# Kernel tuning notes

Hardware: AMD Instinct MI355X
Metric: run time of the kernel (lower is better)

The kernel has to match this reference:

```python
import jax, jax.numpy as jnp
import numpy as np

S = 7
M = 8        # ensemble size (num_models)
D = 1008     # AEV feature dim
N = 50400    # total atoms (single conformer), divisible by S
LAYER_DIMS = (1008, 256, 192, 160, 1)
CELU_ALPHA = 0.1


def setup_inputs() -> dict:
    key = jax.random.key(0)
    ks = jax.random.split(key, 2 + 2 * (len(LAYER_DIMS) - 1))
    # Equal-size species groups (7200 atoms per species), randomly permuted.
    sp = jnp.tile(jnp.arange(S, dtype=jnp.int32), N // S)
    sp = jax.random.permutation(ks[0], sp)[None, :]                 # [1, N]
    aev = jax.random.normal(ks[1], (1, N, D), dtype=jnp.float32)    # [1, N, D]
    inp = {"species": sp, "aev": aev}
    for i in range(len(LAYER_DIMS) - 1):
        fan_in, fan_out = LAYER_DIMS[i], LAYER_DIMS[i + 1]
        w = jax.random.normal(ks[2 + 2 * i], (S, M, fan_in, fan_out), jnp.float32) / np.float32(np.sqrt(fan_in))
        b = jax.random.normal(ks[3 + 2 * i], (S, M, 1, fan_out), jnp.float32) * 0.01
        inp[f"W{i}"] = w
        inp[f"b{i}"] = b
    return inp


def _celu(x, alpha=CELU_ALPHA):
    return jnp.where(x > 0, x, alpha * jnp.expm1(x / alpha))


def _forward(species, aev, Ws, bs):
    sp = species.reshape(-1)                         # [N]
    x = aev.reshape(-1, aev.shape[-1])               # [N, D]
    s = Ws[0].shape[0]
    n = sp.shape[0]
    g = n // s                                       # atoms per species (equal groups)
    # MoE dispatch: stable sort by species -> contiguous equal-size blocks.
    order = jnp.argsort(sp)                          # [N]
    h = x[order].reshape(s, g, -1)                   # [S, G, D]
    # Fused per-species ensemble MLP (grouped batched GEMM = baddbmm per species).
    h = jnp.einsum('sgd,smdh->smgh', h, Ws[0]) + bs[0]   # [S, M, G, H0]
    for w, b in zip(Ws[1:], bs[1:]):
        h = _celu(h)
        h = jnp.einsum('smgh,smhp->smgp', h, w) + b
    atom_e = jnp.mean(h, axis=1)                     # mean over ensemble -> [S, G, 1]
    # Combine: scatter-sum of per-atom energies -> single molecular energy.
    return jnp.sum(atom_e).reshape(1)


def reference(species, aev, W0, b0, W1, b1, W2, b2, W3, b3):
    return _forward(species, aev, (W0, W1, W2, W3), (b0, b1, b2, b3))
```

## Files before the change

### kernel.cpp

```cpp
#include <hip/hip_runtime.h>
#include <cstdint>
#include <cstddef>

typedef unsigned short u16t;
typedef __attribute__((ext_vector_type(8))) short short8;
typedef __attribute__((ext_vector_type(4))) float float4v;

#define NATOMS 50400
#define SSP    7
#define DIN    1008
#define KP     1024
#define GRP    7200
#define GPAD   7296
#define H0D    256
#define H1D    192
#define H2D    160
#define GBSM   28

#define OFF_CNT   0ull
#define OFF_SRC   256ull
#define OFF_X     204544ull
#define OFF_W0T   104800000ull
#define OFF_W1T   134160128ull
#define OFF_W2T   139665152ull
#define OFF_H0    143105792ull

__device__ __forceinline__ u16t f2bf(float f) {
    union { float f; unsigned u; } x; x.f = f;
    unsigned r = x.u + 0x7fffu + ((x.u >> 16) & 1u);
    return (u16t)(r >> 16);
}
__device__ __forceinline__ float bf2f(u16t h) {
    return __uint_as_float(((unsigned)h) << 16);
}
__device__ __forceinline__ float celu_f(float x) {
    return x > 0.f ? x : 0.1f * (__expf(x * 10.f) - 1.f);
}
__device__ __forceinline__ void gll16(const void* g, void* l) {
    __builtin_amdgcn_global_load_lds(
        (const __attribute__((address_space(1))) void*)g,
        (__attribute__((address_space(3))) void*)l, 16, 0, 0);
}


__global__ void assign_k(const int* __restrict__ sp, int* __restrict__ cnt,
                         int* __restrict__ src_of) {
    int i = blockIdx.x * 256 + threadIdx.x;
    int lane = threadIdx.x & 63;
    int s = (i < NATOMS) ? sp[i] : -1;
#pragma unroll
    for (int t = 0; t < SSP; ++t) {
        unsigned long long m = __ballot(s == t);
        if (s == t) {
            int leader = __ffsll((unsigned long long)m) - 1;
            int rank = __popcll(m & ((1ull << lane) - 1ull));
            int base = 0;
            if (lane == leader) base = atomicAdd(&cnt[t], __popcll(m));
            base = __shfl(base, leader);
            src_of[t * GPAD + base + rank] = i;
        }
    }
}

__global__ void gather_k(const float* __restrict__ aev, const int* __restrict__ src_of,
                         u16t* __restrict__ X) {
    int wv = threadIdx.x >> 6, lane = threadIdx.x & 63;
    int s = blockIdx.y;
    int r = blockIdx.x * 4 + wv;
    int b = s * GPAD + r;
    bool valid = (r < GRP);
    int src = valid ? src_of[b] : 0;
    const float* ap = aev + (size_t)src * DIN;
    u16t* xp = X + (size_t)b * KP;
#pragma unroll
    for (int j = 0; j < 4; ++j) {
        int idx = j * 64 + lane;
        int c = idx * 4;
        ushort4 o; o.x = 0; o.y = 0; o.z = 0; o.w = 0;
        if (valid && c < DIN) {
            float4 v = *(const float4*)(ap + c);
            o.x = f2bf(v.x); o.y = f2bf(v.y); o.z = f2bf(v.z); o.w = f2bf(v.w);
        }
        *(ushort4*)(xp + c) = o;
    }
}

__global__ void transpose_convert_k(const float* __restrict__ src, u16t* __restrict__ dst,
                                    int K_in, int C, int K_out) {
    __shared__ float tile[64][65];
    int b = blockIdx.z;
    int k0 = blockIdx.x * 64, c0 = blockIdx.y * 64;
    int tx = threadIdx.x & 63, ty = threadIdx.x >> 6;
    const float* sp = src + (size_t)b * K_in * C;
#pragma unroll
    for (int i = 0; i < 16; ++i) {
        int kl = i * 4 + ty;
        int k = k0 + kl, c = c0 + tx;
        float v = (k < K_in && c < C) ? sp[(size_t)k * C + c] : 0.f;
        tile[kl][tx] = v;
    }
    __syncthreads();
    u16t* dp = dst + (size_t)b * C * K_out;
#pragma unroll
    for (int i = 0; i < 16; ++i) {
        int cl = i * 4 + ty;
        int c = c0 + cl, k = k0 + tx;
        if (c < C && k < K_out)
            dp[(size_t)c * K_out + k] = f2bf(tile[tx][cl]);
    }
}

__launch_bounds__(256, 2)
__global__ void gemm1(const u16t* __restrict__ X, const u16t* __restrict__ W0T,
                      const float* __restrict__ b0, u16t* __restrict__ H0, int bsm0) {
    __shared__ __attribute__((aligned(16))) char lA[16384];
    __shared__ __attribute__((aligned(16))) char lB[32768];

    const int tid = threadIdx.x, w = tid >> 6, lane = tid & 63;
    const int l15 = lane & 15, quad = lane >> 4;
    const int mtile = blockIdx.x >> 1, ntile = blockIdx.x & 1;
    const int by = blockIdx.y;
    const int bsm = bsm0 + by * 2;
    const int s = bsm >> 3;
    const int wr = w & 1, wc = w >> 1;

    const u16t* Xp  = X + ((size_t)s * GPAD + (size_t)mtile * 128) * KP;
    const u16t* Wp0 = W0T + ((size_t)bsm * H0D + (size_t)ntile * 128) * KP;
    const u16t* Wp1 = W0T + ((size_t)(bsm + 1) * H0D + (size_t)ntile * 128) * KP;

    const u16t* gA[4]; const u16t* gB0[4]; const u16t* gB1[4];
#pragma unroll
    for (int j = 0; j < 4; ++j) {
        int u = j * 256 + w * 64 + lane;
        int r = u >> 3;
        int cs = (u & 7) ^ (r & 7);
        size_t off = (size_t)r * KP + cs * 8;
        gA[j]  = Xp  + off;
        gB0[j] = Wp0 + off;
        gB1[j] = Wp1 + off;
    }
    int aoff[4][2], boff[4][2];
#pragma unroll
    for (int rt = 0; rt < 4; ++rt) {
        int r = wr * 64 + rt * 16 + l15;
        int c = wc * 64 + rt * 16 + l15;
#pragma unroll
        for (int ks = 0; ks < 2; ++ks) {
            aoff[rt][ks] = r * 128 + (((ks * 4 + quad) ^ (r & 7)) * 16);
            boff[rt][ks] = c * 128 + (((ks * 4 + quad) ^ (c & 7)) * 16);
        }
    }

    float4v acc[2][4][4];
#pragma unroll
    for (int m = 0; m < 2; ++m)
#pragma unroll
        for (int i = 0; i < 4; ++i)
#pragma unroll
            for (int j = 0; j < 4; ++j) acc[m][i][j] = (float4v){0.f, 0.f, 0.f, 0.f};

    for (int kt = 0; kt < 16; ++kt) {
        const int ko = kt * 64;
        __syncthreads();
#pragma unroll
        for (int j = 0; j < 4; ++j) {
            gll16(gA[j]  + ko, lA + j * 4096 + w * 1024);
            gll16(gB0[j] + ko, lB + j * 4096 + w * 1024);
            gll16(gB1[j] + ko, lB + 16384 + j * 4096 + w * 1024);
        }
        __syncthreads();
#pragma unroll
        for (int ks = 0; ks < 2; ++ks) {
            short8 a[4], b0f[4], b1f[4];
#pragma unroll
            for (int rt = 0; rt < 4; ++rt) a[rt] = *(const short8*)(lA + aoff[rt][ks]);
#pragma unroll
            for (int ct = 0; ct < 4; ++ct) {
                b0f[ct] = *(const short8*)(lB + boff[ct][ks]);
                b1f[ct] = *(const short8*)(lB + 16384 + boff[ct][ks]);
            }
#pragma unroll
            for (int rt = 0; rt < 4; ++rt)
#pragma unroll
                for (int ct = 0; ct < 4; ++ct) {
                    acc[0][rt][ct] = __builtin_amdgcn_mfma_f32_16x16x32_bf16(a[rt], b0f[ct], acc[0][rt][ct], 0, 0, 0);
                    acc[1][rt][ct] = __builtin_amdgcn_mfma_f32_16x16x32_bf16(a[rt], b1f[ct], acc[1][rt][ct], 0, 0, 0);
                }
        }
    }

#pragma unroll
    for (int m = 0; m < 2; ++m) {
        float bias[4];
#pragma unroll
        for (int ct = 0; ct < 4; ++ct)
            bias[ct] = b0[(bsm + m) * H0D + ntile * 128 + wc * 64 + ct * 16 + l15];
        u16t* Hp = H0 + (size_t)(by * 2 + m) * GPAD * H0D;
#pragma unroll
        for (int rt = 0; rt < 4; ++rt)
#pragma unroll
            for (int ct = 0; ct < 4; ++ct) {
                int col = ntile * 128 + wc * 64 + ct * 16 + l15;
#pragma unroll
                for (int rg = 0; rg < 4; ++rg) {
                    int row = mtile * 128 + wr * 64 + rt * 16 + quad * 4 + rg;
                    Hp[(size_t)row * H0D + col] = f2bf(celu_f(acc[m][rt][ct][rg] + bias[ct]));
                }
            }
    }
}

__launch_bounds__(256, 4)
__global__ void mlp234(const u16t* __restrict__ H0, const u16t* __restrict__ W1T,
                       const u16t* __restrict__ W2T, const float* __restrict__ W3,
                       const float* __restrict__ b1, const float* __restrict__ b2,
                       const float* __restrict__ b3, float* __restrict__ out, int bsm0) {
    __shared__ __attribute__((aligned(16))) char lbuf[32768];
    __shared__ float red[4];

    const int tid = threadIdx.x, w = tid >> 6, lane = tid & 63;
    const int l15 = lane & 15, quad = lane >> 4;
    const int by = blockIdx.y, bsm = bsm0 + by;
    const int g0 = blockIdx.x * 64;
    const int wr2 = w & 1, wc2 = w >> 1;

    const u16t* Hg = H0 + ((size_t)by * GPAD + g0) * H0D;
#pragma unroll
    for (int j = 0; j < 8; ++j) {
        int u = j * 256 + w * 64 + lane;
        int r = u >> 5, c5 = u & 31;
        int cs = (c5 & 24) | ((c5 ^ r) & 7);
        gll16(Hg + (size_t)r * H0D + cs * 8, lbuf + j * 4096 + w * 1024);
    }

    const u16t* W1p = W1T + (size_t)bsm * H1D * H0D;
    const u16t* W2p = W2T + (size_t)bsm * H2D * H1D;
    const u16t* bp1[6];
#pragma unroll
    for (int ct = 0; ct < 6; ++ct)
        bp1[ct] = W1p + (size_t)(wc2 * 96 + ct * 16 + l15) * H0D + quad * 8;
    short8 bc[6];
#pragma unroll
    for (int ct = 0; ct < 6; ++ct) bc[ct] = *(const short8*)(bp1[ct]);

    __syncthreads();

    float4v acc2[2][6];
#pragma unroll
    for (int i = 0; i < 2; ++i)
#pragma unroll
        for (int j = 0; j < 6; ++j) acc2[i][j] = (float4v){0.f, 0.f, 0.f, 0.f};

    for (int kc = 0; kc < 8; ++kc) {
        const int kn = ((kc + 1 < 8) ? kc + 1 : kc) * 32;
        short8 a[2];
#pragma unroll
        for (int rt = 0; rt < 2; ++rt) {
            int r = wr2 * 32 + rt * 16 + l15;
            int ch = kc * 4 + quad;
            int sw = (ch & 24) | ((ch ^ r) & 7);
            a[rt] = *(const short8*)(lbuf + r * 512 + sw * 16);
        }
        short8 bn[6];
#pragma unroll
        for (int ct = 0; ct < 6; ++ct) bn[ct] = *(const short8*)(bp1[ct] + kn);
#pragma unroll
        for (int rt = 0; rt < 2; ++rt)
#pragma unroll
            for (int ct = 0; ct < 6; ++ct)
                acc2[rt][ct] = __builtin_amdgcn_mfma_f32_16x16x32_bf16(a[rt], bc[ct], acc2[rt][ct], 0, 0, 0);
#pragma unroll
        for (int ct = 0; ct < 6; ++ct) bc[ct] = bn[ct];
    }

    const u16t* bp2[5];
#pragma unroll
    for (int ct = 0; ct < 5; ++ct)
        bp2[ct] = W2p + (size_t)(wc2 * 80 + ct * 16 + l15) * H1D + quad * 8;
    short8 bc3[5];
#pragma unroll
    for (int ct = 0; ct < 5; ++ct) bc3[ct] = *(const short8*)(bp2[ct]);

    __syncthreads();

    {
        float bias[6];
#pragma unroll
        for (int ct = 0; ct < 6; ++ct) bias[ct] = b1[bsm * H1D + wc2 * 96 + ct * 16 + l15];
#pragma unroll
        for (int rt = 0; rt < 2; ++rt)
#pragma unroll
            for (int ct = 0; ct < 6; ++ct) {
                int h = wc2 * 96 + ct * 16 + l15;
                int ch = h >> 3;
#pragma unroll
                for (int rg = 0; rg < 4; ++rg) {
                    int g = wr2 * 32 + rt * 16 + quad * 4 + rg;
                    float v = celu_f(acc2[rt][ct][rg] + bias[ct]);
                    int sw = (ch & ~7) | ((ch ^ g) & 7);
                    *(u16t*)(lbuf + g * 384 + sw * 16 + (h & 7) * 2) = f2bf(v);
                }
            }
    }
    __syncthreads();

    float4v acc3[2][5];
#pragma unroll
    for (int i = 0; i < 2; ++i)
#pragma unroll
        for (int j = 0; j < 5; ++j) acc3[i][j] = (float4v){0.f, 0.f, 0.f, 0.f};

    for (int kc = 0; kc < 6; ++kc) {
        const int kn = ((kc + 1 < 6) ? kc + 1 : kc) * 32;
        short8 a[2];
#pragma unroll
        for (int rt = 0; rt < 2; ++rt) {
            int r = wr2 * 32 + rt * 16 + l15;
            int ch = kc * 4 + quad;
            int sw = (ch & ~7) | ((ch ^ r) & 7);
            a[rt] = *(const short8*)(lbuf + r * 384 + sw * 16);
        }
        short8 bn[5];
#pragma unroll
        for (int ct = 0; ct < 5; ++ct) bn[ct] = *(const short8*)(bp2[ct] + kn);
#pragma unroll
        for (int rt = 0; rt < 2; ++rt)
#pragma unroll
            for (int ct = 0; ct < 5; ++ct)
                acc3[rt][ct] = __builtin_amdgcn_mfma_f32_16x16x32_bf16(a[rt], bc3[ct], acc3[rt][ct], 0, 0, 0);
#pragma unroll
        for (int ct = 0; ct < 5; ++ct) bc3[ct] = bn[ct];
    }

    {
        float b2r[5], w3r[5];
#pragma unroll
        for (int ct = 0; ct < 5; ++ct) {
            int col = wc2 * 80 + ct * 16 + l15;
            b2r[ct] = b2[bsm * H2D + col];
            w3r[ct] = W3[bsm * H2D + col];
        }
        float s = 0.f;
#pragma unroll
        for (int rt = 0; rt < 2; ++rt)
#pragma unroll
            for (int rg = 0; rg < 4; ++rg) {
                int row = wr2 * 32 + rt * 16 + quad * 4 + rg;
                if (g0 + row < GRP) {
#pragma unroll
                    for (int ct = 0; ct < 5; ++ct)
                        s += celu_f(acc3[rt][ct][rg] + b2r[ct]) * w3r[ct];
                }
            }
#pragma unroll
        for (int off = 32; off; off >>= 1) s += __shfl_xor(s, off);
        if (lane == 0) red[w] = s;
    }
    __syncthreads();
    if (tid == 0) {
        int nv = GRP - g0; nv = nv < 0 ? 0 : (nv > 64 ? 64 : nv);
        atomicAdd(out, (red[0] + red[1] + red[2] + red[3] + (float)nv * b3[bsm]) * 0.125f);
    }
}

extern "C" void kernel_launch(void* const* d_in, const int* in_sizes, int n_in,
                              void* d_out, int out_size, void* d_ws, size_t ws_size,
                              hipStream_t stream) {
    const int*   species = (const int*)d_in[0];
    const float* aev     = (const float*)d_in[1];
    const float* W0      = (const float*)d_in[2];
    const float* b0      = (const float*)d_in[3];
    const float* W1      = (const float*)d_in[4];
    const float* b1      = (const float*)d_in[5];
    const float* W2      = (const float*)d_in[6];
    const float* b2      = (const float*)d_in[7];
    const float* W3      = (const float*)d_in[8];
    const float* b3      = (const float*)d_in[9];
    float* out = (float*)d_out;
    char*  ws  = (char*)d_ws;

    int*  cnt    = (int*)(ws + OFF_CNT);
    int*  src_of = (int*)(ws + OFF_SRC);
    u16t* X      = (u16t*)(ws + OFF_X);
    u16t* W0T    = (u16t*)(ws + OFF_W0T);
    u16t* W1T    = (u16t*)(ws + OFF_W1T);
    u16t* W2T    = (u16t*)(ws + OFF_W2T);
    u16t* H0     = (u16t*)(ws + OFF_H0);

    hipMemsetAsync(cnt, 0, 32, stream);
    hipMemsetAsync(d_out, 0, sizeof(float), stream);

    assign_k<<<(NATOMS + 255) / 256, 256, 0, stream>>>(species, cnt, src_of);
    gather_k<<<dim3(GPAD / 4, SSP), 256, 0, stream>>>(aev, src_of, X);
    transpose_convert_k<<<dim3(16, 4, 56), 256, 0, stream>>>(W0, W0T, DIN, H0D, KP);
    transpose_convert_k<<<dim3(4, 3, 56), 256, 0, stream>>>(W1, W1T, H0D, H1D, H0D);
    transpose_convert_k<<<dim3(3, 3, 56), 256, 0, stream>>>(W2, W2T, H1D, H2D, H1D);

    for (int p = 0; p < 2; ++p) {
        gemm1<<<dim3(114, GBSM / 2), 256, 0, stream>>>(X, W0T, b0, H0, p * GBSM);
        mlp234<<<dim3(114, GBSM), 256, 0, stream>>>(H0, W1T, W2T, W3,
                                                    b1, b2, b3, out, p * GBSM);
    }
}
```

Before: 964.8 us.

## Double-buffer LDS in first-layer GEMM with halved K-tile and prefetch

Restructures the first-layer grouped GEMM mainloop to use two LDS buffers with a K-tile of 32 instead of 64. The next tile's global-to-LDS loads are issued before the MFMAs on the current tile, and one barrier per iteration replaces two. The goal is to hide global load latency behind matrix math. In exchange the swizzle pattern changes, the iteration count doubles, and LDS use stays at 48KB.

```diff
diff --git a/kernel.cpp b/kernel.cpp
--- a/kernel.cpp
+++ b/kernel.cpp
@@ -113,8 +113,7 @@
 __launch_bounds__(256, 2)
 __global__ void gemm1(const u16t* __restrict__ X, const u16t* __restrict__ W0T,
                       const float* __restrict__ b0, u16t* __restrict__ H0, int bsm0) {
-    __shared__ __attribute__((aligned(16))) char lA[16384];
-    __shared__ __attribute__((aligned(16))) char lB[32768];
+    __shared__ __attribute__((aligned(16))) char lds[49152];
 
     const int tid = threadIdx.x, w = tid >> 6, lane = tid & 63;
     const int l15 = lane & 15, quad = lane >> 4;
@@ -128,27 +127,23 @@
     const u16t* Wp0 = W0T + ((size_t)bsm * H0D + (size_t)ntile * 128) * KP;
     const u16t* Wp1 = W0T + ((size_t)(bsm + 1) * H0D + (size_t)ntile * 128) * KP;
 
-    const u16t* gA[4]; const u16t* gB0[4]; const u16t* gB1[4];
-#pragma unroll
-    for (int j = 0; j < 4; ++j) {
-        int u = j * 256 + w * 64 + lane;
-        int r = u >> 3;
-        int cs = (u & 7) ^ (r & 7);
+    const u16t* gA[2]; const u16t* gB0[2]; const u16t* gB1[2];
+#pragma unroll
+    for (int j = 0; j < 2; ++j) {
+        int u = j * 256 + tid;
+        int r = u >> 2;
+        int cs = (u & 3) ^ (r & 3);
         size_t off = (size_t)r * KP + cs * 8;
         gA[j]  = Xp  + off;
         gB0[j] = Wp0 + off;
         gB1[j] = Wp1 + off;
     }
-    int aoff[4][2], boff[4][2];
-#pragma unroll
-    for (int rt = 0; rt < 4; ++rt) {
-        int r = wr * 64 + rt * 16 + l15;
-        int c = wc * 64 + rt * 16 + l15;
-#pragma unroll
-        for (int ks = 0; ks < 2; ++ks) {
-            aoff[rt][ks] = r * 128 + (((ks * 4 + quad) ^ (r & 7)) * 16);
-            boff[rt][ks] = c * 128 + (((ks * 4 + quad) ^ (c & 7)) * 16);
-        }
+    const int chv = (quad ^ (l15 & 3)) * 16;
+    int aoff[4], boff[4];
+#pragma unroll
+    for (int t = 0; t < 4; ++t) {
+        aoff[t] = (wr * 64 + t * 16 + l15) * 64 + chv;
+        boff[t] = (wc * 64 + t * 16 + l15) * 64 + chv;
     }
 
     float4v acc[2][4][4];
@@ -159,34 +154,47 @@
 #pragma unroll
             for (int j = 0; j < 4; ++j) acc[m][i][j] = (float4v){0.f, 0.f, 0.f, 0.f};
 
-    for (int kt = 0; kt < 16; ++kt) {
-        const int ko = kt * 64;
+    {
+        char* base = lds;
+#pragma unroll
+        for (int j = 0; j < 2; ++j) {
+            gll16(gA[j],  base + j * 4096 + w * 1024);
+            gll16(gB0[j], base + 8192  + j * 4096 + w * 1024);
+            gll16(gB1[j], base + 16384 + j * 4096 + w * 1024);
+        }
+    }
+    __syncthreads();
+
+    int cur = 0;
+    for (int kt = 0; kt < 32; ++kt) {
+        const char* bp = lds + cur * 24576;
+        short8 a[4], b0f[4], b1f[4];
+#pragma unroll
+        for (int rt = 0; rt < 4; ++rt) a[rt] = *(const short8*)(bp + aoff[rt]);
+#pragma unroll
+        for (int ct = 0; ct < 4; ++ct) {
+            b0f[ct] = *(const short8*)(bp + 8192  + boff[ct]);
+            b1f[ct] = *(const short8*)(bp + 16384 + boff[ct]);
+        }
+        if (kt < 31) {
+            char* base = lds + (cur ^ 1) * 24576;
+            const int ko = (kt + 1) * 32;
+#pragma unroll
+            for (int j = 0; j < 2; ++j) {
+                gll16(gA[j]  + ko, base + j * 4096 + w * 1024);
+                gll16(gB0[j] + ko, base + 8192  + j * 4096 + w * 1024);
+                gll16(gB1[j] + ko, base + 16384 + j * 4096 + w * 1024);
+            }
+        }
+#pragma unroll
+        for (int rt = 0; rt < 4; ++rt)
+#pragma unroll
+            for (int ct = 0; ct < 4; ++ct) {
+                acc[0][rt][ct] = __builtin_amdgcn_mfma_f32_16x16x32_bf16(a[rt], b0f[ct], acc[0][rt][ct], 0, 0, 0);
+                acc[1][rt][ct] = __builtin_amdgcn_mfma_f32_16x16x32_bf16(a[rt], b1f[ct], acc[1][rt][ct], 0, 0, 0);
+            }
         __syncthreads();
-#pragma unroll
-        for (int j = 0; j < 4; ++j) {
-            gll16(gA[j]  + ko, lA + j * 4096 + w * 1024);
-            gll16(gB0[j] + ko, lB + j * 4096 + w * 1024);
-            gll16(gB1[j] + ko, lB + 16384 + j * 4096 + w * 1024);
-        }
-        __syncthreads();
-#pragma unroll
-        for (int ks = 0; ks < 2; ++ks) {
-            short8 a[4], b0f[4], b1f[4];
-#pragma unroll
-            for (int rt = 0; rt < 4; ++rt) a[rt] = *(const short8*)(lA + aoff[rt][ks]);
-#pragma unroll
-            for (int ct = 0; ct < 4; ++ct) {
-                b0f[ct] = *(const short8*)(lB + boff[ct][ks]);
-                b1f[ct] = *(const short8*)(lB + 16384 + boff[ct][ks]);
-            }
-#pragma unroll
-            for (int rt = 0; rt < 4; ++rt)
-#pragma unroll
-                for (int ct = 0; ct < 4; ++ct) {
-                    acc[0][rt][ct] = __builtin_amdgcn_mfma_f32_16x16x32_bf16(a[rt], b0f[ct], acc[0][rt][ct], 0, 0, 0);
-                    acc[1][rt][ct] = __builtin_amdgcn_mfma_f32_16x16x32_bf16(a[rt], b1f[ct], acc[1][rt][ct], 0, 0, 0);
-                }
-        }
+        cur ^= 1;
     }
 
 #pragma unroll
```

New measurement: 997.5 us. +3.4%, slower.
